# Performance work log

Hardware: AMD Instinct MI355X
Metric: run time of the kernel (lower is better)

Reference implementation:

```python
import jax, jax.numpy as jnp
import numpy as np

I_P = 8  # input_patch == output_patch


def extract_patches(x, i_p=I_P):
    # x: (B, N, C, H, W) -> (r, N*i_p*i_p, B, C), matching nn.Unfold(i_p, 1, 0, i_p)
    # followed by rearrange '(b n) (c i) r -> r (n i) b c' with i = h*w row-major.
    B, N, C, H, W = x.shape
    s1, s2 = H // i_p, W // i_p
    p = x.reshape(B, N, C, s1, i_p, s2, i_p)
    p = jnp.transpose(p, (3, 5, 1, 4, 6, 0, 2))  # (s1, s2, N, ph, pw, B, C)
    return p.reshape(s1 * s2, N * i_p * i_p, B, C)


def setup_inputs() -> dict:
    key = jax.random.key(0)
    ks = jax.random.split(key, 8)
    B, N, C, H = 1, 5, 3, 256
    inputs = jax.random.normal(ks[0], (B, N, C, H, H), jnp.float32)
    outputs = jax.random.normal(ks[1], (B, N, C, H, H), jnp.float32)
    # q/k projections of nn.MultiheadAttention(3, 1); v_proj and out_proj are frozen identity.
    Wq = jax.random.normal(ks[2], (3, 3), jnp.float32) * 0.5
    Wk = jax.random.normal(ks[3], (3, 3), jnp.float32) * 0.5
    bq = jax.random.normal(ks[4], (3,), jnp.float32) * 0.05
    bk = jax.random.normal(ks[5], (3,), jnp.float32) * 0.05
    bv = jnp.zeros((3,), jnp.float32)  # in_proj_bias for v initialised to zero
    return {
        "inputs": inputs,
        "outputs": outputs,
        "Wq": Wq,
        "Wk": Wk,
        "bq": bq,
        "bk": bk,
        "bv": bv,
        "loss_diff": jnp.float32(0.5),
        "step": 10,
        "max_steps": 100,
    }


def reference(inputs, outputs, Wq, Wk, bq, bk, bv, loss_diff, step, max_steps):
    B, N, C, H, W = inputs.shape
    i_p = I_P
    s = H // i_p
    mid = N // 2

    # (r, L, 3) with L = N*i_p^2; batch dim B==1 squeezed.
    X = extract_patches(inputs)[:, :, 0, :]
    Y = extract_patches(outputs)[:, :, 0, :]

    # The per-frame attention calls concatenated over frames equal a single
    # self-attention with Q=K=V=in_patches_flat (softmax is row-wise in queries).
    q = (X @ Wq.T + bq) / jnp.sqrt(jnp.float32(3.0))  # head_dim = 3
    k = X @ Wk.T + bk
    v = X + bv  # v_proj is identity (frozen)
    scores = jnp.einsum("rld,rmd->rlm", q, k)          # (r, L, L)
    attn = jax.nn.softmax(scores, axis=-1)
    out = jnp.einsum("rlm,rmd->rld", attn, v)           # out_proj identity, bias 0

    r = out.shape[0]
    # '(n h w) bs d -> (bs n) d h w' with bs=1  ->  (r, N, 3, i_p, i_p)
    align = out.reshape(r, N, i_p, i_p, 3).transpose(0, 1, 4, 2, 3)
    nin = Y.reshape(r, N, i_p, i_p, 3).transpose(0, 1, 4, 2, 3)

    per_patch_mse = lambda a, b: jnp.mean((a - b) ** 2, axis=(1, 2, 3, 4))
    mid_loss = jnp.sum(per_patch_mse(jnp.broadcast_to(nin[:, mid:mid + 1], align.shape), align))
    all_loss = jnp.sum(per_patch_mse(nin, align))
    coeff = loss_diff * (1.0 - step / max_steps) ** 10

    rec = jnp.mean(align, axis=1)  # (r, 3, i_p, i_p)
    rec_image = rec.reshape(s, s, 3, i_p, i_p).transpose(2, 0, 3, 1, 4).reshape(1, 3, H, W)
    rec_loss = jnp.mean((outputs[:, mid] - rec_image) ** 2)

    loss = mid_loss + coeff * all_loss + rec_loss
    return loss, rec_image
```

## Files before the change

### kernel.cpp

```cpp
#include <hip/hip_runtime.h>

#define HW    256
#define PLANE (256*256)
#define MID   2
#define NF    5
#define VTS   328

typedef float f32x4 __attribute__((ext_vector_type(4)));
typedef short s16x8 __attribute__((ext_vector_type(8)));

__device__ __forceinline__ float hw_exp2(float x) {
#if __has_builtin(__builtin_amdgcn_exp2f)
    return __builtin_amdgcn_exp2f(x);
#else
    float r; asm("v_exp_f32 %0, %1" : "=v"(r) : "v"(x)); return r;
#endif
}

__device__ __forceinline__ unsigned int f2bf(float f) {
    unsigned int u = __float_as_uint(f);
    u += 0x7FFF + ((u >> 16) & 1);
    return u >> 16;
}

__device__ __forceinline__ unsigned int pack_bf(float a, float b) {
    return __builtin_amdgcn_perm(__float_as_uint(b), __float_as_uint(a), 0x07060302u);
}

__device__ __forceinline__ s16x8 mk_frag4(uint2 lo) {
    union { s16x8 v; unsigned int u[4]; } c;
    c.u[0] = lo.x; c.u[1] = lo.y; c.u[2] = 0; c.u[3] = 0;
    return c.v;
}
__device__ __forceinline__ s16x8 mk_frag8(unsigned int u0, unsigned int u1,
                                          unsigned int u2, unsigned int u3) {
    union { s16x8 v; unsigned int u[4]; } c;
    c.u[0] = u0; c.u[1] = u1; c.u[2] = u2; c.u[3] = u3;
    return c.v;
}

__global__ __launch_bounds__(256) void attn_mfma_kernel(
    const float* __restrict__ in,
    const float* __restrict__ outp,
    const float* __restrict__ Wq,
    const float* __restrict__ Wk,
    const float* __restrict__ bq,
    const float* __restrict__ bk,
    const float* __restrict__ bv,
    const float* __restrict__ loss_diff,
    const int*   __restrict__ step,
    const int*   __restrict__ max_steps,
    float* __restrict__ d_out)
{
    __shared__ __align__(16) unsigned short Kbf[324 * 4];
    __shared__ __align__(16) unsigned short Qbf[320 * 4];
    __shared__ __align__(16) unsigned short Vt[16 * VTS];
    __shared__ __align__(16) float oLDS[320 * 4];
    __shared__ float red[4];

    const int tid  = threadIdx.x;
    const int w    = tid >> 6;
    const int lane = tid & 63;
    const int col  = lane & 15;
    const int quad = lane >> 4;
    const int r    = blockIdx.x;
    const int s1   = r >> 5, s2 = r & 31;

    {
        unsigned int* v32 = (unsigned int*)Vt;
        for (int idx = 3 * (VTS / 2) + tid; idx < 16 * (VTS / 2); idx += 256)
            v32[idx] = (idx < 4 * (VTS / 2)) ? 0x3F803F80u : 0u;
    }
    if (tid < 4) *(uint2*)&Kbf[(320 + tid) * 4] = make_uint2(0u, 0u);

    const float QS = 0.57735026918962576f * 1.44269504088896340f;
    const float bv0 = bv[0], bv1 = bv[1], bv2 = bv[2];
    for (int t = tid; t < 320; t += 256) {
        const int n = t >> 6, i = t & 63;
        const int pix = (s1 * 8 + (i >> 3)) * HW + s2 * 8 + (i & 7);
        const float x0 = in[(n * 3 + 0) * PLANE + pix];
        const float x1 = in[(n * 3 + 1) * PLANE + pix];
        const float x2 = in[(n * 3 + 2) * PLANE + pix];
        const float k0 = x0 * Wk[0] + x1 * Wk[1] + x2 * Wk[2] + bk[0];
        const float k1 = x0 * Wk[3] + x1 * Wk[4] + x2 * Wk[5] + bk[1];
        const float k2 = x0 * Wk[6] + x1 * Wk[7] + x2 * Wk[8] + bk[2];
        const float q0 = (x0 * Wq[0] + x1 * Wq[1] + x2 * Wq[2] + bq[0]) * QS;
        const float q1 = (x0 * Wq[3] + x1 * Wq[4] + x2 * Wq[5] + bq[1]) * QS;
        const float q2 = (x0 * Wq[6] + x1 * Wq[7] + x2 * Wq[8] + bq[2]) * QS;
        *(uint2*)&Kbf[t * 4] = make_uint2(f2bf(k0) | (f2bf(k1) << 16), f2bf(k2));
        *(uint2*)&Qbf[t * 4] = make_uint2(f2bf(q0) | (f2bf(q1) << 16), f2bf(q2));
        Vt[0 * VTS + t] = (unsigned short)f2bf(x0 + bv0);
        Vt[1 * VTS + t] = (unsigned short)f2bf(x1 + bv1);
        Vt[2 * VTS + t] = (unsigned short)f2bf(x2 + bv2);
    }

    const int nA = tid >> 6, iA = tid & 63;
    const int pixA = (s1 * 8 + (iA >> 3)) * HW + s2 * 8 + (iA & 7);
    const float yA0  = outp[(nA * 3 + 0) * PLANE + pixA];
    const float yA1  = outp[(nA * 3 + 1) * PLANE + pixA];
    const float yA2  = outp[(nA * 3 + 2) * PLANE + pixA];
    const float ymA0 = outp[(MID * 3 + 0) * PLANE + pixA];
    const float ymA1 = outp[(MID * 3 + 1) * PLANE + pixA];
    const float ymA2 = outp[(MID * 3 + 2) * PLANE + pixA];
    const int tB = (tid < 64) ? tid + 256 : tid;
    const int nB = tB >> 6, iB = tB & 63;
    const int pixB = (s1 * 8 + (iB >> 3)) * HW + s2 * 8 + (iB & 7);
    const float yB0  = outp[(nB * 3 + 0) * PLANE + pixB];
    const float yB1  = outp[(nB * 3 + 1) * PLANE + pixB];
    const float yB2  = outp[(nB * 3 + 2) * PLANE + pixB];
    const float ymB0 = outp[(MID * 3 + 0) * PLANE + pixB];
    const float ymB1 = outp[(MID * 3 + 1) * PLANE + pixB];
    const float ymB2 = outp[(MID * 3 + 2) * PLANE + pixB];
    __syncthreads();

    s16x8 qf[5];
#pragma unroll
    for (int u = 0; u < 5; ++u) {
        uint2 qr = *(const uint2*)&Qbf[((w * 5 + u) * 16 + col) * 4];
        if (quad != 0) { qr.x = 0; qr.y = 0; }
        qf[u] = mk_frag4(qr);
    }

    f32x4 acc[5];
#pragma unroll
    for (int u = 0; u < 5; ++u) acc[u] = (f32x4){0.f, 0.f, 0.f, 0.f};
    const f32x4 zero4 = (f32x4){0.f, 0.f, 0.f, 0.f};

    const bool kz = (quad == 0);
#pragma unroll 2
    for (int kb = 0; kb < 10; ++kb) {
        const int i0 = kz ? (kb * 32 + col) : 320;
        const int i1 = kz ? (kb * 32 + 16 + col) : 320;
        const s16x8 a0 = mk_frag4(*(const uint2*)&Kbf[i0 * 4]);
        const s16x8 a1 = mk_frag4(*(const uint2*)&Kbf[i1 * 4]);
        const unsigned short* vp = &Vt[col * VTS + kb * 32 + quad * 4];
        const uint2 vlo = *(const uint2*)vp;
        const uint2 vhi = *(const uint2*)(vp + 16);
        const s16x8 vf = mk_frag8(vlo.x, vlo.y, vhi.x, vhi.y);
#pragma unroll
        for (int u = 0; u < 5; ++u) {
            f32x4 c0 = __builtin_amdgcn_mfma_f32_16x16x32_bf16(a0, qf[u], zero4, 0, 0, 0);
            f32x4 c1 = __builtin_amdgcn_mfma_f32_16x16x32_bf16(a1, qf[u], zero4, 0, 0, 0);
            const unsigned int p0 = pack_bf(hw_exp2(c0[0]), hw_exp2(c0[1]));
            const unsigned int p1 = pack_bf(hw_exp2(c0[2]), hw_exp2(c0[3]));
            const unsigned int p2 = pack_bf(hw_exp2(c1[0]), hw_exp2(c1[1]));
            const unsigned int p3 = pack_bf(hw_exp2(c1[2]), hw_exp2(c1[3]));
            const s16x8 pf = mk_frag8(p0, p1, p2, p3);
            acc[u] = __builtin_amdgcn_mfma_f32_16x16x32_bf16(pf, vf, acc[u], 0, 0, 0);
        }
    }

    if (col < 4) {
#pragma unroll
        for (int u = 0; u < 5; ++u) {
            const int tbase = (w * 5 + u) * 16 + quad * 4;
#pragma unroll
            for (int rr = 0; rr < 4; ++rr)
                oLDS[(tbase + rr) * 4 + col] = acc[u][rr];
        }
    }
    __syncthreads();

    float tl = 0.0f;
    const float tt = 1.0f - (float)step[0] / (float)max_steps[0];
    const float t2 = tt * tt, t4 = t2 * t2, t8 = t4 * t4;
    const float coeff = loss_diff[0] * t8 * t2;

    {
        const float4 oa = *(const float4*)&oLDS[tid * 4];
        const float inv = 1.0f / oa.w;
        const float o0 = oa.x * inv, o1 = oa.y * inv, o2 = oa.z * inv;
        const float d0 = ymA0 - o0, d1 = ymA1 - o1, d2 = ymA2 - o2;
        const float e0 = yA0 - o0,  e1 = yA1 - o1,  e2 = yA2 - o2;
        tl += (d0*d0 + d1*d1 + d2*d2 + coeff * (e0*e0 + e1*e1 + e2*e2)) * (1.0f / 960.0f);
    }
    if (tid < 64) {
        const float4 oa = *(const float4*)&oLDS[(tid + 256) * 4];
        const float inv = 1.0f / oa.w;
        const float o0 = oa.x * inv, o1 = oa.y * inv, o2 = oa.z * inv;
        const float d0 = ymB0 - o0, d1 = ymB1 - o1, d2 = ymB2 - o2;
        const float e0 = yB0 - o0,  e1 = yB1 - o1,  e2 = yB2 - o2;
        tl += (d0*d0 + d1*d1 + d2*d2 + coeff * (e0*e0 + e1*e1 + e2*e2)) * (1.0f / 960.0f);
    }

    if (tid < 192) {
        const int c = tid >> 6;
        float rec = 0.0f;
#pragma unroll
        for (int n = 0; n < NF; ++n) {
            const int t = n * 64 + iA;
            rec += oLDS[t * 4 + c] / oLDS[t * 4 + 3];
        }
        rec *= 0.2f;
        d_out[1 + c * PLANE + pixA] = rec;
        const float ym = (c == 0) ? ymA0 : ((c == 1) ? ymA1 : ymA2);
        const float dr = ym - rec;
        tl += dr * dr * (1.0f / 196608.0f);
    }

#pragma unroll
    for (int off = 32; off; off >>= 1) tl += __shfl_down(tl, off);
    if (lane == 0) red[w] = tl;
    __syncthreads();
    if (tid == 0) atomicAdd(d_out, red[0] + red[1] + red[2] + red[3]);
}

extern "C" void kernel_launch(void* const* d_in, const int* in_sizes, int n_in,
                              void* d_out, int out_size, void* d_ws, size_t ws_size,
                              hipStream_t stream) {
    const float* in        = (const float*)d_in[0];
    const float* outp      = (const float*)d_in[1];
    const float* Wq        = (const float*)d_in[2];
    const float* Wk        = (const float*)d_in[3];
    const float* bq        = (const float*)d_in[4];
    const float* bk        = (const float*)d_in[5];
    const float* bv        = (const float*)d_in[6];
    const float* loss_diff = (const float*)d_in[7];
    const int*   step      = (const int*)d_in[8];
    const int*   max_steps = (const int*)d_in[9];
    float* out = (float*)d_out;

    hipMemsetAsync(out, 0, sizeof(float), stream);

    attn_mfma_kernel<<<1024, 256, 0, stream>>>(
        in, outp, Wq, Wk, bq, bk, bv, loss_diff, step, max_steps, out);
}
```

Baseline: 100.8 us.

## Split attention keys across two blocks per patch and finalize in separate kernel

Each patch's key/value range is now divided between two blocks, which doubles the grid to 2048 blocks. Each block writes unnormalized partial numerators and denominators to workspace, and a second kernel sums the halves, normalizes, and computes the losses and the reconstructed image. The aim is more parallelism and less per-block serial exp/MFMA work. The cost is an extra kernel launch, a workspace round trip through global memory, and Q projection repeated in both halves.

After: 116.2 us. 15.2% more time.

```diff
diff --git a/kernel.cpp b/kernel.cpp
--- a/kernel.cpp
+++ b/kernel.cpp
@@ -4,7 +4,7 @@
 #define PLANE (256*256)
 #define MID   2
 #define NF    5
-#define VTS   328
+#define VTS2  168
 
 typedef float f32x4 __attribute__((ext_vector_type(4)));
 typedef short s16x8 __attribute__((ext_vector_type(8)));
@@ -39,44 +39,53 @@
     return c.v;
 }
 
-__global__ __launch_bounds__(256) void attn_mfma_kernel(
+__global__ __launch_bounds__(256) void attn_partial_mfma(
     const float* __restrict__ in,
-    const float* __restrict__ outp,
     const float* __restrict__ Wq,
     const float* __restrict__ Wk,
     const float* __restrict__ bq,
     const float* __restrict__ bk,
     const float* __restrict__ bv,
-    const float* __restrict__ loss_diff,
-    const int*   __restrict__ step,
-    const int*   __restrict__ max_steps,
-    float* __restrict__ d_out)
+    float* __restrict__ ws)
 {
-    __shared__ __align__(16) unsigned short Kbf[324 * 4];
+    __shared__ __align__(16) unsigned short Kbf[164 * 4];
     __shared__ __align__(16) unsigned short Qbf[320 * 4];
-    __shared__ __align__(16) unsigned short Vt[16 * VTS];
-    __shared__ __align__(16) float oLDS[320 * 4];
-    __shared__ float red[4];
+    __shared__ __align__(16) unsigned short Vt[16 * VTS2];
 
     const int tid  = threadIdx.x;
     const int w    = tid >> 6;
     const int lane = tid & 63;
     const int col  = lane & 15;
     const int quad = lane >> 4;
-    const int r    = blockIdx.x;
+    const int b    = blockIdx.x;
+    const int r    = b >> 1;
+    const int h    = b & 1;
     const int s1   = r >> 5, s2 = r & 31;
 
     {
         unsigned int* v32 = (unsigned int*)Vt;
-        for (int idx = 3 * (VTS / 2) + tid; idx < 16 * (VTS / 2); idx += 256)
-            v32[idx] = (idx < 4 * (VTS / 2)) ? 0x3F803F80u : 0u;
-    }
-    if (tid < 4) *(uint2*)&Kbf[(320 + tid) * 4] = make_uint2(0u, 0u);
+        for (int idx = 3 * (VTS2 / 2) + tid; idx < 16 * (VTS2 / 2); idx += 256)
+            v32[idx] = (idx < 4 * (VTS2 / 2)) ? 0x3F803F80u : 0u;
+    }
+    if (tid < 4) *(uint2*)&Kbf[(160 + tid) * 4] = make_uint2(0u, 0u);
 
     const float QS = 0.57735026918962576f * 1.44269504088896340f;
     const float bv0 = bv[0], bv1 = bv[1], bv2 = bv[2];
+
     for (int t = tid; t < 320; t += 256) {
         const int n = t >> 6, i = t & 63;
+        const int pix = (s1 * 8 + (i >> 3)) * HW + s2 * 8 + (i & 7);
+        const float x0 = in[(n * 3 + 0) * PLANE + pix];
+        const float x1 = in[(n * 3 + 1) * PLANE + pix];
+        const float x2 = in[(n * 3 + 2) * PLANE + pix];
+        const float q0 = (x0 * Wq[0] + x1 * Wq[1] + x2 * Wq[2] + bq[0]) * QS;
+        const float q1 = (x0 * Wq[3] + x1 * Wq[4] + x2 * Wq[5] + bq[1]) * QS;
+        const float q2 = (x0 * Wq[6] + x1 * Wq[7] + x2 * Wq[8] + bq[2]) * QS;
+        *(uint2*)&Qbf[t * 4] = make_uint2(f2bf(q0) | (f2bf(q1) << 16), f2bf(q2));
+    }
+    if (tid < 160) {
+        const int g = h * 160 + tid;
+        const int n = g >> 6, i = g & 63;
         const int pix = (s1 * 8 + (i >> 3)) * HW + s2 * 8 + (i & 7);
         const float x0 = in[(n * 3 + 0) * PLANE + pix];
         const float x1 = in[(n * 3 + 1) * PLANE + pix];
@@ -84,33 +93,11 @@
         const float k0 = x0 * Wk[0] + x1 * Wk[1] + x2 * Wk[2] + bk[0];
         const float k1 = x0 * Wk[3] + x1 * Wk[4] + x2 * Wk[5] + bk[1];
         const float k2 = x0 * Wk[6] + x1 * Wk[7] + x2 * Wk[8] + bk[2];
-        const float q0 = (x0 * Wq[0] + x1 * Wq[1] + x2 * Wq[2] + bq[0]) * QS;
-        const float q1 = (x0 * Wq[3] + x1 * Wq[4] + x2 * Wq[5] + bq[1]) * QS;
-        const float q2 = (x0 * Wq[6] + x1 * Wq[7] + x2 * Wq[8] + bq[2]) * QS;
-        *(uint2*)&Kbf[t * 4] = make_uint2(f2bf(k0) | (f2bf(k1) << 16), f2bf(k2));
-        *(uint2*)&Qbf[t * 4] = make_uint2(f2bf(q0) | (f2bf(q1) << 16), f2bf(q2));
-        Vt[0 * VTS + t] = (unsigned short)f2bf(x0 + bv0);
-        Vt[1 * VTS + t] = (unsigned short)f2bf(x1 + bv1);
-        Vt[2 * VTS + t] = (unsigned short)f2bf(x2 + bv2);
-    }
-
-    const int nA = tid >> 6, iA = tid & 63;
-    const int pixA = (s1 * 8 + (iA >> 3)) * HW + s2 * 8 + (iA & 7);
-    const float yA0  = outp[(nA * 3 + 0) * PLANE + pixA];
-    const float yA1  = outp[(nA * 3 + 1) * PLANE + pixA];
-    const float yA2  = outp[(nA * 3 + 2) * PLANE + pixA];
-    const float ymA0 = outp[(MID * 3 + 0) * PLANE + pixA];
-    const float ymA1 = outp[(MID * 3 + 1) * PLANE + pixA];
-    const float ymA2 = outp[(MID * 3 + 2) * PLANE + pixA];
-    const int tB = (tid < 64) ? tid + 256 : tid;
-    const int nB = tB >> 6, iB = tB & 63;
-    const int pixB = (s1 * 8 + (iB >> 3)) * HW + s2 * 8 + (iB & 7);
-    const float yB0  = outp[(nB * 3 + 0) * PLANE + pixB];
-    const float yB1  = outp[(nB * 3 + 1) * PLANE + pixB];
-    const float yB2  = outp[(nB * 3 + 2) * PLANE + pixB];
-    const float ymB0 = outp[(MID * 3 + 0) * PLANE + pixB];
-    const float ymB1 = outp[(MID * 3 + 1) * PLANE + pixB];
-    const float ymB2 = outp[(MID * 3 + 2) * PLANE + pixB];
+        *(uint2*)&Kbf[tid * 4] = make_uint2(f2bf(k0) | (f2bf(k1) << 16), f2bf(k2));
+        Vt[0 * VTS2 + tid] = (unsigned short)f2bf(x0 + bv0);
+        Vt[1 * VTS2 + tid] = (unsigned short)f2bf(x1 + bv1);
+        Vt[2 * VTS2 + tid] = (unsigned short)f2bf(x2 + bv2);
+    }
     __syncthreads();
 
     s16x8 qf[5];
@@ -128,12 +115,12 @@
 
     const bool kz = (quad == 0);
 #pragma unroll 2
-    for (int kb = 0; kb < 10; ++kb) {
-        const int i0 = kz ? (kb * 32 + col) : 320;
-        const int i1 = kz ? (kb * 32 + 16 + col) : 320;
+    for (int kb = 0; kb < 5; ++kb) {
+        const int i0 = kz ? (kb * 32 + col) : 160;
+        const int i1 = kz ? (kb * 32 + 16 + col) : 160;
         const s16x8 a0 = mk_frag4(*(const uint2*)&Kbf[i0 * 4]);
         const s16x8 a1 = mk_frag4(*(const uint2*)&Kbf[i1 * 4]);
-        const unsigned short* vp = &Vt[col * VTS + kb * 32 + quad * 4];
+        const unsigned short* vp = &Vt[col * VTS2 + kb * 32 + quad * 4];
         const uint2 vlo = *(const uint2*)vp;
         const uint2 vhi = *(const uint2*)(vp + 16);
         const s16x8 vf = mk_frag8(vlo.x, vlo.y, vhi.x, vhi.y);
@@ -151,58 +138,77 @@
     }
 
     if (col < 4) {
+        const int base = b * 320;
 #pragma unroll
         for (int u = 0; u < 5; ++u) {
             const int tbase = (w * 5 + u) * 16 + quad * 4;
 #pragma unroll
             for (int rr = 0; rr < 4; ++rr)
-                oLDS[(tbase + rr) * 4 + col] = acc[u][rr];
+                ws[(base + tbase + rr) * 4 + col] = acc[u][rr];
         }
     }
-    __syncthreads();
-
-    float tl = 0.0f;
-    const float tt = 1.0f - (float)step[0] / (float)max_steps[0];
-    const float t2 = tt * tt, t4 = t2 * t2, t8 = t4 * t4;
+}
+
+__global__ __launch_bounds__(256) void finalize_kernel(
+    const float* __restrict__ outp,
+    const float* __restrict__ loss_diff,
+    const int*   __restrict__ step,
+    const int*   __restrict__ max_steps,
+    const float4* __restrict__ ws4,
+    float* __restrict__ d_out)
+{
+    const int tid = threadIdx.x;
+    const int w   = tid >> 6;
+    const int l   = tid & 63;
+    const int r   = blockIdx.x * 4 + w;
+    const int s1  = r >> 5, s2 = r & 31;
+    const int pix = (s1 * 8 + (l >> 3)) * HW + s2 * 8 + (l & 7);
+
+    float o[NF][3];
+#pragma unroll
+    for (int j = 0; j < NF; ++j) {
+        const float4 pa = ws4[(2 * r)     * 320 + j * 64 + l];
+        const float4 pb = ws4[(2 * r + 1) * 320 + j * 64 + l];
+        const float inv = 1.0f / (pa.w + pb.w);
+        o[j][0] = (pa.x + pb.x) * inv;
+        o[j][1] = (pa.y + pb.y) * inv;
+        o[j][2] = (pa.z + pb.z) * inv;
+    }
+
+    float y[NF][3];
+#pragma unroll
+    for (int j = 0; j < NF; ++j)
+#pragma unroll
+        for (int c = 0; c < 3; ++c)
+            y[j][c] = outp[(j * 3 + c) * PLANE + pix];
+
+    const float t  = 1.0f - (float)step[0] / (float)max_steps[0];
+    const float t2 = t * t, t4 = t2 * t2, t8 = t4 * t4;
     const float coeff = loss_diff[0] * t8 * t2;
 
-    {
-        const float4 oa = *(const float4*)&oLDS[tid * 4];
-        const float inv = 1.0f / oa.w;
-        const float o0 = oa.x * inv, o1 = oa.y * inv, o2 = oa.z * inv;
-        const float d0 = ymA0 - o0, d1 = ymA1 - o1, d2 = ymA2 - o2;
-        const float e0 = yA0 - o0,  e1 = yA1 - o1,  e2 = yA2 - o2;
-        tl += (d0*d0 + d1*d1 + d2*d2 + coeff * (e0*e0 + e1*e1 + e2*e2)) * (1.0f / 960.0f);
-    }
-    if (tid < 64) {
-        const float4 oa = *(const float4*)&oLDS[(tid + 256) * 4];
-        const float inv = 1.0f / oa.w;
-        const float o0 = oa.x * inv, o1 = oa.y * inv, o2 = oa.z * inv;
-        const float d0 = ymB0 - o0, d1 = ymB1 - o1, d2 = ymB2 - o2;
-        const float e0 = yB0 - o0,  e1 = yB1 - o1,  e2 = yB2 - o2;
-        tl += (d0*d0 + d1*d1 + d2*d2 + coeff * (e0*e0 + e1*e1 + e2*e2)) * (1.0f / 960.0f);
-    }
-
-    if (tid < 192) {
-        const int c = tid >> 6;
-        float rec = 0.0f;
-#pragma unroll
-        for (int n = 0; n < NF; ++n) {
-            const int t = n * 64 + iA;
-            rec += oLDS[t * 4 + c] / oLDS[t * 4 + 3];
+    float midp = 0.0f, allp = 0.0f;
+#pragma unroll
+    for (int j = 0; j < NF; ++j)
+#pragma unroll
+        for (int c = 0; c < 3; ++c) {
+            const float d = y[MID][c] - o[j][c];
+            const float e = y[j][c]   - o[j][c];
+            midp += d * d;
+            allp += e * e;
         }
-        rec *= 0.2f;
-        d_out[1 + c * PLANE + pixA] = rec;
-        const float ym = (c == 0) ? ymA0 : ((c == 1) ? ymA1 : ymA2);
-        const float dr = ym - rec;
+    float tl = (midp + coeff * allp) * (1.0f / 960.0f);
+
+#pragma unroll
+    for (int c = 0; c < 3; ++c) {
+        const float rec = 0.2f * (o[0][c] + o[1][c] + o[2][c] + o[3][c] + o[4][c]);
+        d_out[1 + c * PLANE + pix] = rec;
+        const float dr = y[MID][c] - rec;
         tl += dr * dr * (1.0f / 196608.0f);
     }
 
 #pragma unroll
     for (int off = 32; off; off >>= 1) tl += __shfl_down(tl, off);
-    if (lane == 0) red[w] = tl;
-    __syncthreads();
-    if (tid == 0) atomicAdd(d_out, red[0] + red[1] + red[2] + red[3]);
+    if (l == 0) atomicAdd(d_out, tl);
 }
 
 extern "C" void kernel_launch(void* const* d_in, const int* in_sizes, int n_in,
@@ -219,9 +225,11 @@
     const int*   step      = (const int*)d_in[8];
     const int*   max_steps = (const int*)d_in[9];
     float* out = (float*)d_out;
+    float* ws  = (float*)d_ws;
 
     hipMemsetAsync(out, 0, sizeof(float), stream);
 
-    attn_mfma_kernel<<<1024, 256, 0, stream>>>(
-        in, outp, Wq, Wk, bq, bk, bv, loss_diff, step, max_steps, out);
-}
+    attn_partial_mfma<<<2048, 256, 0, stream>>>(in, Wq, Wk, bq, bk, bv, ws);
+    finalize_kernel<<<256, 256, 0, stream>>>(outp, loss_diff, step, max_steps,
+                                             (const float4*)ws, out);
+}
```
